# Optimization experiments

Measured on AMD Instinct MI355X. Metric: run time of the kernel, lower is better.

Reference implementation:

```python
import jax, jax.numpy as jnp
import numpy as np

N, C, K = 100000, 64, 27
EPS = 1e-5


def setup_inputs() -> dict:
    key = jax.random.key(0)
    ks = jax.random.split(key, 8)
    feats = jax.random.normal(ks[0], (N, C), dtype=jnp.float32)
    W1 = jax.random.normal(ks[1], (K, C, C), dtype=jnp.float32) * (1.0 / np.sqrt(K * C))
    W2 = jax.random.normal(ks[2], (K, C, C), dtype=jnp.float32) * (1.0 / np.sqrt(K * C))
    gamma1 = jnp.ones((C,), dtype=jnp.float32)
    beta1 = jnp.zeros((C,), dtype=jnp.float32)
    gamma2 = jnp.ones((C,), dtype=jnp.float32)
    beta2 = jnp.zeros((C,), dtype=jnp.float32)
    nbr_idx1 = jax.random.randint(ks[3], (K, N), 0, N, dtype=jnp.int32)
    nbr_idx2 = jax.random.randint(ks[4], (K, N), 0, N, dtype=jnp.int32)
    nbr_mask1 = (jax.random.uniform(ks[5], (K, N)) < 0.7).astype(jnp.float32)
    nbr_mask2 = (jax.random.uniform(ks[6], (K, N)) < 0.7).astype(jnp.float32)
    return {"feats": feats, "W1": W1, "gamma1": gamma1, "beta1": beta1,
            "W2": W2, "gamma2": gamma2, "beta2": beta2,
            "nbr_idx1": nbr_idx1, "nbr_mask1": nbr_mask1,
            "nbr_idx2": nbr_idx2, "nbr_mask2": nbr_mask2}


def sparse_conv(f, idx, mask, W):
    # gather per kernel offset: [K, N, C], mask out missing neighbors
    g = f[idx] * mask[..., None]
    # per-offset GEMM and accumulate over offsets -> [N, C_out]
    return jnp.einsum('knc,kcd->nd', g, W)


def batch_norm(x, gamma, beta):
    # MinkowskiBatchNorm (training): stats over all N points, per channel
    mean = jnp.mean(x, axis=0)
    var = jnp.mean(jnp.square(x - mean), axis=0)
    return (x - mean) * jax.lax.rsqrt(var + EPS) * gamma + beta


def reference(feats, W1, gamma1, beta1, W2, gamma2, beta2,
              nbr_idx1, nbr_mask1, nbr_idx2, nbr_mask2):
    out = sparse_conv(feats, nbr_idx1, nbr_mask1, W1)
    out = jax.nn.relu(batch_norm(out, gamma1, beta1))
    out = sparse_conv(out, nbr_idx2, nbr_mask2, W2)
    out = batch_norm(out, gamma2, beta2)
    out = out + feats          # identity residual (stride=1, no downsample)
    return jax.nn.relu(out)
```

## Files before the change

kernel.cpp:

```cpp
#include <hip/hip_runtime.h>
#include <hip/hip_bf16.h>
#include <stdint.h>
#include <stddef.h>

#define N_PTS 100000
#define KOFF 27

typedef __attribute__((ext_vector_type(8))) __bf16 bf16x8;
typedef __attribute__((ext_vector_type(16))) float f32x16;

__device__ inline unsigned short f2bf(float f) {
  union { float f; unsigned u; } x; x.f = f;
  unsigned r = x.u + 0x7fffu + ((x.u >> 16) & 1u);
  return (unsigned short)(r >> 16);
}

__global__ void fprep_kernel(const float* __restrict__ feats,
                             unsigned short* __restrict__ featsb,
                             unsigned short* __restrict__ f2b,
                             float* __restrict__ stats) {
  int tid = blockIdx.x * blockDim.x + threadIdx.x;
  int stride = gridDim.x * blockDim.x;
  const int NF4 = N_PTS * 16;
  for (int i = tid; i < NF4; i += stride) {
    float4 v = ((const float4*)feats)[i];
    ushort4 o;
    o.x = f2bf(v.x); o.y = f2bf(v.y); o.z = f2bf(v.z); o.w = f2bf(v.w);
    ((ushort4*)featsb)[i] = o;
  }
  if (tid < 256) stats[tid] = 0.f;
  if (tid >= 256 && tid < 264) {
    uint4 z = make_uint4(0u, 0u, 0u, 0u);
    ((uint4*)(featsb + (size_t)N_PTS * 64))[tid - 256] = z;
  }
  if (tid >= 264 && tid < 272) {
    uint4 z = make_uint4(0u, 0u, 0u, 0u);
    ((uint4*)(f2b + (size_t)N_PTS * 64))[tid - 264] = z;
  }
}

__global__ __launch_bounds__(256) void wprep_kernel(const float* __restrict__ W1,
                                                    const float* __restrict__ W2,
                                                    unsigned short* __restrict__ wf1,
                                                    unsigned short* __restrict__ wf2) {
  __shared__ float sW[4096];
  int which = blockIdx.x & 1;
  int k = blockIdx.x >> 1;
  const float* W = (which ? W2 : W1) + (size_t)k * 4096;
  unsigned short* wf = (which ? wf2 : wf1) + (size_t)k * 4096;
  int t = threadIdx.x;
#pragma unroll
  for (int i = 0; i < 4; ++i) {
    ((float4*)sW)[t + 256 * i] = ((const float4*)W)[t + 256 * i];
  }
  __syncthreads();
#pragma unroll
  for (int i = 0; i < 16; ++i) {
    int o = i * 256 + t;
    int j = o & 7, l = (o >> 3) & 63, ct = (o >> 9) & 1, ks = o >> 10;
    int c = ks * 16 + ((l >> 5) << 3) + j;
    int d = (ct << 5) + (l & 31);
    wf[o] = f2bf(sW[c * 64 + d]);
  }
}

#define MFMA(a, b, c) __builtin_amdgcn_mfma_f32_32x32x16_bf16(__builtin_bit_cast(bf16x8, a), __builtin_bit_cast(bf16x8, b), c, 0, 0, 0)

#define STEP(Ac, Bc, An, Bn, giN, mN, giF, mF, kcur)                         \
  {                                                                          \
    int gie = (mN != 0.f) ? giN : N_PTS;                                     \
    const uint4* ar = (const uint4*)(fin + (size_t)gie * 64);                \
    An[0] = ar[hi]; An[1] = ar[2 + hi]; An[2] = ar[4 + hi]; An[3] = ar[6 + hi]; \
    {                                                                        \
      int kn = ((kcur) + 1 <= 26) ? (kcur) + 1 : 26;                         \
      const uint4* bp = wfv + (size_t)kn * 512 + lane;                       \
      Bn[0] = bp[0];   Bn[1] = bp[64];  Bn[2] = bp[128]; Bn[3] = bp[192];    \
      Bn[4] = bp[256]; Bn[5] = bp[320]; Bn[6] = bp[384]; Bn[7] = bp[448];    \
    }                                                                        \
    {                                                                        \
      int kf = ((kcur) + 2 <= 26) ? (kcur) + 2 : 26;                         \
      giF = idxp[kf * N_PTS];                                                \
      float mt = mp[kf * N_PTS];                                             \
      mF = valid ? mt : 0.f;                                                 \
    }                                                                        \
    acc0 = MFMA(Ac[0], Bc[0], acc0);                                         \
    acc1 = MFMA(Ac[0], Bc[1], acc1);                                         \
    acc0 = MFMA(Ac[1], Bc[2], acc0);                                         \
    acc1 = MFMA(Ac[1], Bc[3], acc1);                                         \
    acc0 = MFMA(Ac[2], Bc[4], acc0);                                         \
    acc1 = MFMA(Ac[2], Bc[5], acc1);                                         \
    acc0 = MFMA(Ac[3], Bc[6], acc0);                                         \
    acc1 = MFMA(Ac[3], Bc[7], acc1);                                         \
  }

__global__ __launch_bounds__(256, 3) void conv_kernel(
    const unsigned short* __restrict__ fin,
    const unsigned short* __restrict__ wf,
    const int* __restrict__ idx,
    const float* __restrict__ mask,
    float* __restrict__ yout,
    float* __restrict__ gsum,
    float* __restrict__ gsq)
{
  int lane = threadIdx.x & 63;
  int wid  = threadIdx.x >> 6;
  int col  = lane & 31;
  int hi   = lane >> 5;
  int n0   = blockIdx.x * 128 + wid * 32;
  int n    = n0 + col;
  bool valid = n < N_PTS;
  int nc = valid ? n : (N_PTS - 1);

  const int*   idxp = idx + nc;
  const float* mp   = mask + nc;
  const uint4* wfv  = (const uint4*)wf;

  f32x16 acc0, acc1;
#pragma unroll
  for (int r = 0; r < 16; ++r) { acc0[r] = 0.f; acc1[r] = 0.f; }

  uint4 A0[4], A1[4], B0[8], B1[8];
  int gi0, gi1; float m0, m1;

  gi0 = idxp[0];
  { float mt = mp[0]; m0 = valid ? mt : 0.f; }
  {
    int gie = (m0 != 0.f) ? gi0 : N_PTS;
    const uint4* ar = (const uint4*)(fin + (size_t)gie * 64);
    A0[0] = ar[hi]; A0[1] = ar[2 + hi]; A0[2] = ar[4 + hi]; A0[3] = ar[6 + hi];
    const uint4* bp = wfv + lane;
    B0[0] = bp[0];   B0[1] = bp[64];  B0[2] = bp[128]; B0[3] = bp[192];
    B0[4] = bp[256]; B0[5] = bp[320]; B0[6] = bp[384]; B0[7] = bp[448];
  }
  gi1 = idxp[N_PTS];
  { float mt = mp[N_PTS]; m1 = valid ? mt : 0.f; }

  for (int kk = 0; kk < 13; ++kk) {
    int k = 2 * kk;
    STEP(A0, B0, A1, B1, gi1, m1, gi0, m0, k);
    STEP(A1, B1, A0, B0, gi0, m0, gi1, m1, k + 1);
  }
  acc0 = MFMA(A0[0], B0[0], acc0);
  acc1 = MFMA(A0[0], B0[1], acc1);
  acc0 = MFMA(A0[1], B0[2], acc0);
  acc1 = MFMA(A0[1], B0[3], acc1);
  acc0 = MFMA(A0[2], B0[4], acc0);
  acc1 = MFMA(A0[2], B0[5], acc1);
  acc0 = MFMA(A0[3], B0[6], acc0);
  acc1 = MFMA(A0[3], B0[7], acc1);

  __shared__ float s_sum[64], s_sq[64];
  if (threadIdx.x < 64) { s_sum[threadIdx.x] = 0.f; s_sq[threadIdx.x] = 0.f; }
  __syncthreads();

  float s0 = 0.f, q0 = 0.f, s1 = 0.f, q1 = 0.f;
#pragma unroll
  for (int r = 0; r < 16; ++r) {
    float v = acc0[r]; s0 += v; q0 += v * v;
    float w = acc1[r]; s1 += w; q1 += w * w;
    int rr = (r & 3) + ((r >> 2) << 3) + (hi << 2);
    int nr = n0 + rr;
    if (nr < N_PTS) {
      yout[(size_t)nr * 64 + col]      = v;
      yout[(size_t)nr * 64 + 32 + col] = w;
    }
  }
  atomicAdd(&s_sum[col], s0);
  atomicAdd(&s_sq[col],  q0);
  atomicAdd(&s_sum[32 + col], s1);
  atomicAdd(&s_sq[32 + col],  q1);
  __syncthreads();
  if (threadIdx.x < 64) {
    atomicAdd(&gsum[threadIdx.x], s_sum[threadIdx.x]);
    atomicAdd(&gsq[threadIdx.x],  s_sq[threadIdx.x]);
  }
}

__global__ void bn1_kernel(const float* __restrict__ y,
                           const float* __restrict__ sum,
                           const float* __restrict__ sq,
                           const float* __restrict__ gamma,
                           const float* __restrict__ beta,
                           unsigned short* __restrict__ outb) {
  __shared__ float s_scale[64], s_shift[64];
  if (threadIdx.x < 64) {
    int c = threadIdx.x;
    float mean = sum[c] * (1.f / N_PTS);
    float var  = sq[c] * (1.f / N_PTS) - mean * mean;
    float inv  = rsqrtf(var + 1e-5f);
    float sc   = gamma[c] * inv;
    s_scale[c] = sc;
    s_shift[c] = beta[c] - mean * sc;
  }
  __syncthreads();
  int tid = blockIdx.x * blockDim.x + threadIdx.x;
  int stride = gridDim.x * blockDim.x;
  const int NT = N_PTS * 16;
  for (int i = tid; i < NT; i += stride) {
    float4 v = ((const float4*)y)[i];
    int c = (i * 4) & 63;
    float r0 = fmaxf(v.x * s_scale[c]     + s_shift[c],     0.f);
    float r1 = fmaxf(v.y * s_scale[c + 1] + s_shift[c + 1], 0.f);
    float r2 = fmaxf(v.z * s_scale[c + 2] + s_shift[c + 2], 0.f);
    float r3 = fmaxf(v.w * s_scale[c + 3] + s_shift[c + 3], 0.f);
    ushort4 o;
    o.x = f2bf(r0); o.y = f2bf(r1); o.z = f2bf(r2); o.w = f2bf(r3);
    ((ushort4*)outb)[i] = o;
  }
}

__global__ void bn2_kernel(const float* __restrict__ y,
                           const float* __restrict__ sum,
                           const float* __restrict__ sq,
                           const float* __restrict__ gamma,
                           const float* __restrict__ beta,
                           const float* __restrict__ feats,
                           float* __restrict__ out) {
  __shared__ float s_scale[64], s_shift[64];
  if (threadIdx.x < 64) {
    int c = threadIdx.x;
    float mean = sum[c] * (1.f / N_PTS);
    float var  = sq[c] * (1.f / N_PTS) - mean * mean;
    float inv  = rsqrtf(var + 1e-5f);
    float sc   = gamma[c] * inv;
    s_scale[c] = sc;
    s_shift[c] = beta[c] - mean * sc;
  }
  __syncthreads();
  int tid = blockIdx.x * blockDim.x + threadIdx.x;
  int stride = gridDim.x * blockDim.x;
  const int NT = N_PTS * 16;
  for (int i = tid; i < NT; i += stride) {
    float4 v = ((const float4*)y)[i];
    float4 f = ((const float4*)feats)[i];
    int c = (i * 4) & 63;
    float4 o;
    o.x = fmaxf(v.x * s_scale[c]     + s_shift[c]     + f.x, 0.f);
    o.y = fmaxf(v.y * s_scale[c + 1] + s_shift[c + 1] + f.y, 0.f);
    o.z = fmaxf(v.z * s_scale[c + 2] + s_shift[c + 2] + f.z, 0.f);
    o.w = fmaxf(v.w * s_scale[c + 3] + s_shift[c + 3] + f.w, 0.f);
    ((float4*)out)[i] = o;
  }
}

extern "C" void kernel_launch(void* const* d_in, const int* in_sizes, int n_in,
                              void* d_out, int out_size, void* d_ws, size_t ws_size,
                              hipStream_t stream) {
  const float* feats  = (const float*)d_in[0];
  const float* W1     = (const float*)d_in[1];
  const float* gamma1 = (const float*)d_in[2];
  const float* beta1  = (const float*)d_in[3];
  const float* W2     = (const float*)d_in[4];
  const float* gamma2 = (const float*)d_in[5];
  const float* beta2  = (const float*)d_in[6];
  const int*   idx1   = (const int*)d_in[7];
  const float* mask1  = (const float*)d_in[8];
  const int*   idx2   = (const int*)d_in[9];
  const float* mask2  = (const float*)d_in[10];
  float* out = (float*)d_out;

  char* ws = (char*)d_ws;
  unsigned short* featsb = (unsigned short*)(ws + 0);
  unsigned short* wf1    = (unsigned short*)(ws + 12800768);
  unsigned short* wf2    = (unsigned short*)(ws + 13021952);
  float*          stats  = (float*)(ws + 13243136);
  unsigned short* f2b    = (unsigned short*)(ws + 13244160);

  float* sum1 = stats;       float* sq1 = stats + 64;
  float* sum2 = stats + 128; float* sq2 = stats + 192;

  float* y = out;

  fprep_kernel<<<1024, 256, 0, stream>>>(feats, featsb, f2b, stats);
  wprep_kernel<<<54, 256, 0, stream>>>(W1, W2, wf1, wf2);

  const int CONV_GRID = (N_PTS + 127) / 128;
  conv_kernel<<<CONV_GRID, 256, 0, stream>>>(featsb, wf1, idx1, mask1, y, sum1, sq1);
  bn1_kernel<<<1024, 256, 0, stream>>>(y, sum1, sq1, gamma1, beta1, f2b);
  conv_kernel<<<CONV_GRID, 256, 0, stream>>>(f2b, wf2, idx2, mask2, y, sum2, sq2);
  bn2_kernel<<<1024, 256, 0, stream>>>(y, sum2, sq2, gamma2, beta2, feats, out);
}
```

Measured before the change: 335.1 us.

## Switch conv to 16x16x32 MFMA tiles with 16-point waves and fused prep kernel

```diff
diff --git a/kernel.cpp b/kernel.cpp
--- a/kernel.cpp
+++ b/kernel.cpp
@@ -7,7 +7,7 @@
 #define KOFF 27
 
 typedef __attribute__((ext_vector_type(8))) __bf16 bf16x8;
-typedef __attribute__((ext_vector_type(16))) float f32x16;
+typedef __attribute__((ext_vector_type(4))) float f32x4;
 
 __device__ inline unsigned short f2bf(float f) {
   union { float f; unsigned u; } x; x.f = f;
@@ -15,85 +15,82 @@
   return (unsigned short)(r >> 16);
 }
 
-__global__ void fprep_kernel(const float* __restrict__ feats,
-                             unsigned short* __restrict__ featsb,
-                             unsigned short* __restrict__ f2b,
-                             float* __restrict__ stats) {
-  int tid = blockIdx.x * blockDim.x + threadIdx.x;
-  int stride = gridDim.x * blockDim.x;
+__global__ __launch_bounds__(256) void prep_kernel(const float* __restrict__ feats,
+                                                   const float* __restrict__ W1,
+                                                   const float* __restrict__ W2,
+                                                   unsigned short* __restrict__ featsb,
+                                                   unsigned short* __restrict__ f2b,
+                                                   unsigned short* __restrict__ wf1,
+                                                   unsigned short* __restrict__ wf2,
+                                                   float* __restrict__ stats) {
+  __shared__ float sW[4096];
+  int t = threadIdx.x;
+  if (blockIdx.x < 54) {
+    int which = blockIdx.x & 1;
+    int k = blockIdx.x >> 1;
+    const float* W = (which ? W2 : W1) + (size_t)k * 4096;
+    unsigned short* wf = (which ? wf2 : wf1) + (size_t)k * 4096;
+#pragma unroll
+    for (int i = 0; i < 4; ++i)
+      ((float4*)sW)[t + 256 * i] = ((const float4*)W)[t + 256 * i];
+    __syncthreads();
+#pragma unroll
+    for (int i = 0; i < 16; ++i) {
+      int o = i * 256 + t;
+      int j = o & 7, l = (o >> 3) & 63, nt = (o >> 9) & 3, kk = (o >> 11) & 1;
+      int c = kk * 32 + ((l >> 4) << 3) + j;
+      int d = nt * 16 + (l & 15);
+      wf[o] = f2bf(sW[c * 64 + d]);
+    }
+    return;
+  }
+  int fb = blockIdx.x - 54;
+  int NB = gridDim.x - 54;
   const int NF4 = N_PTS * 16;
-  for (int i = tid; i < NF4; i += stride) {
+  for (int i = fb * 256 + t; i < NF4; i += NB * 256) {
     float4 v = ((const float4*)feats)[i];
     ushort4 o;
     o.x = f2bf(v.x); o.y = f2bf(v.y); o.z = f2bf(v.z); o.w = f2bf(v.w);
     ((ushort4*)featsb)[i] = o;
   }
-  if (tid < 256) stats[tid] = 0.f;
-  if (tid >= 256 && tid < 264) {
+  if (fb == 0) {
+    if (t < 256) stats[t] = 0.f;
     uint4 z = make_uint4(0u, 0u, 0u, 0u);
-    ((uint4*)(featsb + (size_t)N_PTS * 64))[tid - 256] = z;
-  }
-  if (tid >= 264 && tid < 272) {
-    uint4 z = make_uint4(0u, 0u, 0u, 0u);
-    ((uint4*)(f2b + (size_t)N_PTS * 64))[tid - 264] = z;
-  }
-}
-
-__global__ __launch_bounds__(256) void wprep_kernel(const float* __restrict__ W1,
-                                                    const float* __restrict__ W2,
-                                                    unsigned short* __restrict__ wf1,
-                                                    unsigned short* __restrict__ wf2) {
-  __shared__ float sW[4096];
-  int which = blockIdx.x & 1;
-  int k = blockIdx.x >> 1;
-  const float* W = (which ? W2 : W1) + (size_t)k * 4096;
-  unsigned short* wf = (which ? wf2 : wf1) + (size_t)k * 4096;
-  int t = threadIdx.x;
-#pragma unroll
-  for (int i = 0; i < 4; ++i) {
-    ((float4*)sW)[t + 256 * i] = ((const float4*)W)[t + 256 * i];
-  }
-  __syncthreads();
-#pragma unroll
-  for (int i = 0; i < 16; ++i) {
-    int o = i * 256 + t;
-    int j = o & 7, l = (o >> 3) & 63, ct = (o >> 9) & 1, ks = o >> 10;
-    int c = ks * 16 + ((l >> 5) << 3) + j;
-    int d = (ct << 5) + (l & 31);
-    wf[o] = f2bf(sW[c * 64 + d]);
-  }
-}
-
-#define MFMA(a, b, c) __builtin_amdgcn_mfma_f32_32x32x16_bf16(__builtin_bit_cast(bf16x8, a), __builtin_bit_cast(bf16x8, b), c, 0, 0, 0)
-
-#define STEP(Ac, Bc, An, Bn, giN, mN, giF, mF, kcur)                         \
-  {                                                                          \
-    int gie = (mN != 0.f) ? giN : N_PTS;                                     \
-    const uint4* ar = (const uint4*)(fin + (size_t)gie * 64);                \
-    An[0] = ar[hi]; An[1] = ar[2 + hi]; An[2] = ar[4 + hi]; An[3] = ar[6 + hi]; \
-    {                                                                        \
-      int kn = ((kcur) + 1 <= 26) ? (kcur) + 1 : 26;                         \
-      const uint4* bp = wfv + (size_t)kn * 512 + lane;                       \
-      Bn[0] = bp[0];   Bn[1] = bp[64];  Bn[2] = bp[128]; Bn[3] = bp[192];    \
-      Bn[4] = bp[256]; Bn[5] = bp[320]; Bn[6] = bp[384]; Bn[7] = bp[448];    \
-    }                                                                        \
-    {                                                                        \
-      int kf = ((kcur) + 2 <= 26) ? (kcur) + 2 : 26;                         \
-      giF = idxp[kf * N_PTS];                                                \
-      float mt = mp[kf * N_PTS];                                             \
-      mF = valid ? mt : 0.f;                                                 \
-    }                                                                        \
-    acc0 = MFMA(Ac[0], Bc[0], acc0);                                         \
-    acc1 = MFMA(Ac[0], Bc[1], acc1);                                         \
-    acc0 = MFMA(Ac[1], Bc[2], acc0);                                         \
-    acc1 = MFMA(Ac[1], Bc[3], acc1);                                         \
-    acc0 = MFMA(Ac[2], Bc[4], acc0);                                         \
-    acc1 = MFMA(Ac[2], Bc[5], acc1);                                         \
-    acc0 = MFMA(Ac[3], Bc[6], acc0);                                         \
-    acc1 = MFMA(Ac[3], Bc[7], acc1);                                         \
-  }
-
-__global__ __launch_bounds__(256, 3) void conv_kernel(
+    if (t < 8)            ((uint4*)(featsb + (size_t)N_PTS * 64))[t] = z;
+    if (t >= 8 && t < 16) ((uint4*)(f2b    + (size_t)N_PTS * 64))[t - 8] = z;
+  }
+}
+
+#define MFMA16(a, b, c) __builtin_amdgcn_mfma_f32_16x16x32_bf16(__builtin_bit_cast(bf16x8, a), __builtin_bit_cast(bf16x8, b), c, 0, 0, 0)
+
+#define STEP(Ac0, Ac1, An0, An1, giN, mN, giF, mF, kcur)                        \
+  {                                                                             \
+    const uint4* bp = wfv + (size_t)(kcur) * 512 + lane;                        \
+    uint4 b0 = bp[0],   b1 = bp[64],  b2 = bp[128], b3 = bp[192];               \
+    uint4 b4 = bp[256], b5 = bp[320], b6 = bp[384], b7 = bp[448];               \
+    {                                                                           \
+      int gie = (mN != 0.f) ? giN : N_PTS;                                      \
+      const char* rp = (const char*)fin + (size_t)gie * 128 + g16;              \
+      An0 = *(const uint4*)rp;                                                  \
+      An1 = *(const uint4*)(rp + 64);                                           \
+    }                                                                           \
+    {                                                                           \
+      int kf = ((kcur) + 2 <= 26) ? (kcur) + 2 : 26;                            \
+      giF = idxp[(size_t)kf * N_PTS];                                           \
+      float mt = mp[(size_t)kf * N_PTS];                                        \
+      mF = valid ? mt : 0.f;                                                    \
+    }                                                                           \
+    a0 = MFMA16(Ac0, b0, a0);                                                   \
+    a1 = MFMA16(Ac0, b1, a1);                                                   \
+    a2 = MFMA16(Ac0, b2, a2);                                                   \
+    a3 = MFMA16(Ac0, b3, a3);                                                   \
+    a0 = MFMA16(Ac1, b4, a0);                                                   \
+    a1 = MFMA16(Ac1, b5, a1);                                                   \
+    a2 = MFMA16(Ac1, b6, a2);                                                   \
+    a3 = MFMA16(Ac1, b7, a3);                                                   \
+  }
+
+__global__ __launch_bounds__(256, 4) void conv_kernel(
     const unsigned short* __restrict__ fin,
     const unsigned short* __restrict__ wf,
     const int* __restrict__ idx,
@@ -104,10 +101,11 @@
 {
   int lane = threadIdx.x & 63;
   int wid  = threadIdx.x >> 6;
-  int col  = lane & 31;
-  int hi   = lane >> 5;
-  int n0   = blockIdx.x * 128 + wid * 32;
-  int n    = n0 + col;
+  int m    = lane & 15;
+  int g    = lane >> 4;
+  int g16  = g * 16;
+  int n0   = blockIdx.x * 64 + wid * 16;
+  int n    = n0 + m;
   bool valid = n < N_PTS;
   int nc = valid ? n : (N_PTS - 1);
 
@@ -115,60 +113,68 @@
   const float* mp   = mask + nc;
   const uint4* wfv  = (const uint4*)wf;
 
-  f32x16 acc0, acc1;
-#pragma unroll
-  for (int r = 0; r < 16; ++r) { acc0[r] = 0.f; acc1[r] = 0.f; }
-
-  uint4 A0[4], A1[4], B0[8], B1[8];
-  int gi0, gi1; float m0, m1;
-
-  gi0 = idxp[0];
-  { float mt = mp[0]; m0 = valid ? mt : 0.f; }
+  f32x4 a0, a1, a2, a3;
+#pragma unroll
+  for (int r = 0; r < 4; ++r) { a0[r] = 0.f; a1[r] = 0.f; a2[r] = 0.f; a3[r] = 0.f; }
+
+  uint4 Aa0, Aa1, Ab0, Ab1;
+  int gi_a, gi_b; float m_a, m_b;
+
+  gi_a = idxp[0];
+  { float mt = mp[0]; m_a = valid ? mt : 0.f; }
   {
-    int gie = (m0 != 0.f) ? gi0 : N_PTS;
-    const uint4* ar = (const uint4*)(fin + (size_t)gie * 64);
-    A0[0] = ar[hi]; A0[1] = ar[2 + hi]; A0[2] = ar[4 + hi]; A0[3] = ar[6 + hi];
-    const uint4* bp = wfv + lane;
-    B0[0] = bp[0];   B0[1] = bp[64];  B0[2] = bp[128]; B0[3] = bp[192];
-    B0[4] = bp[256]; B0[5] = bp[320]; B0[6] = bp[384]; B0[7] = bp[448];
-  }
-  gi1 = idxp[N_PTS];
-  { float mt = mp[N_PTS]; m1 = valid ? mt : 0.f; }
+    int gie = (m_a != 0.f) ? gi_a : N_PTS;
+    const char* rp = (const char*)fin + (size_t)gie * 128 + g16;
+    Aa0 = *(const uint4*)rp;
+    Aa1 = *(const uint4*)(rp + 64);
+  }
+  gi_b = idxp[N_PTS];
+  { float mt = mp[N_PTS]; m_b = valid ? mt : 0.f; }
 
   for (int kk = 0; kk < 13; ++kk) {
     int k = 2 * kk;
-    STEP(A0, B0, A1, B1, gi1, m1, gi0, m0, k);
-    STEP(A1, B1, A0, B0, gi0, m0, gi1, m1, k + 1);
-  }
-  acc0 = MFMA(A0[0], B0[0], acc0);
-  acc1 = MFMA(A0[0], B0[1], acc1);
-  acc0 = MFMA(A0[1], B0[2], acc0);
-  acc1 = MFMA(A0[1], B0[3], acc1);
-  acc0 = MFMA(A0[2], B0[4], acc0);
-  acc1 = MFMA(A0[2], B0[5], acc1);
-  acc0 = MFMA(A0[3], B0[6], acc0);
-  acc1 = MFMA(A0[3], B0[7], acc1);
+    STEP(Aa0, Aa1, Ab0, Ab1, gi_b, m_b, gi_a, m_a, k);
+    STEP(Ab0, Ab1, Aa0, Aa1, gi_a, m_a, gi_b, m_b, k + 1);
+  }
+  {
+    const uint4* bp = wfv + (size_t)26 * 512 + lane;
+    uint4 b0 = bp[0],   b1 = bp[64],  b2 = bp[128], b3 = bp[192];
+    uint4 b4 = bp[256], b5 = bp[320], b6 = bp[384], b7 = bp[448];
+    a0 = MFMA16(Aa0, b0, a0);
+    a1 = MFMA16(Aa0, b1, a1);
+    a2 = MFMA16(Aa0, b2, a2);
+    a3 = MFMA16(Aa0, b3, a3);
+    a0 = MFMA16(Aa1, b4, a0);
+    a1 = MFMA16(Aa1, b5, a1);
+    a2 = MFMA16(Aa1, b6, a2);
+    a3 = MFMA16(Aa1, b7, a3);
+  }
 
   __shared__ float s_sum[64], s_sq[64];
   if (threadIdx.x < 64) { s_sum[threadIdx.x] = 0.f; s_sq[threadIdx.x] = 0.f; }
   __syncthreads();
 
-  float s0 = 0.f, q0 = 0.f, s1 = 0.f, q1 = 0.f;
-#pragma unroll
-  for (int r = 0; r < 16; ++r) {
-    float v = acc0[r]; s0 += v; q0 += v * v;
-    float w = acc1[r]; s1 += w; q1 += w * w;
-    int rr = (r & 3) + ((r >> 2) << 3) + (hi << 2);
-    int nr = n0 + rr;
-    if (nr < N_PTS) {
-      yout[(size_t)nr * 64 + col]      = v;
-      yout[(size_t)nr * 64 + 32 + col] = w;
+  float s0 = 0.f, q0 = 0.f, s1 = 0.f, q1 = 0.f, s2 = 0.f, q2 = 0.f, s3 = 0.f, q3 = 0.f;
+#pragma unroll
+  for (int r = 0; r < 4; ++r) {
+    int row = n0 + g * 4 + r;
+    bool rv = row < N_PTS;
+    float v0 = a0[r]; s0 += v0; q0 += v0 * v0;
+    float v1 = a1[r]; s1 += v1; q1 += v1 * v1;
+    float v2 = a2[r]; s2 += v2; q2 += v2 * v2;
+    float v3 = a3[r]; s3 += v3; q3 += v3 * v3;
+    if (rv) {
+      float* yr = yout + (size_t)row * 64;
+      yr[m]      = v0;
+      yr[16 + m] = v1;
+      yr[32 + m] = v2;
+      yr[48 + m] = v3;
     }
   }
-  atomicAdd(&s_sum[col], s0);
-  atomicAdd(&s_sq[col],  q0);
-  atomicAdd(&s_sum[32 + col], s1);
-  atomicAdd(&s_sq[32 + col],  q1);
+  atomicAdd(&s_sum[m],      s0); atomicAdd(&s_sq[m],      q0);
+  atomicAdd(&s_sum[16 + m], s1); atomicAdd(&s_sq[16 + m], q1);
+  atomicAdd(&s_sum[32 + m], s2); atomicAdd(&s_sq[32 + m], q2);
+  atomicAdd(&s_sum[48 + m], s3); atomicAdd(&s_sq[48 + m], q3);
   __syncthreads();
   if (threadIdx.x < 64) {
     atomicAdd(&gsum[threadIdx.x], s_sum[threadIdx.x]);
@@ -271,10 +277,9 @@
 
   float* y = out;
 
-  fprep_kernel<<<1024, 256, 0, stream>>>(feats, featsb, f2b, stats);
-  wprep_kernel<<<54, 256, 0, stream>>>(W1, W2, wf1, wf2);
-
-  const int CONV_GRID = (N_PTS + 127) / 128;
+  prep_kernel<<<54 + 640, 256, 0, stream>>>(feats, W1, W2, featsb, f2b, wf1, wf2, stats);
+
+  const int CONV_GRID = (N_PTS + 63) / 64;
   conv_kernel<<<CONV_GRID, 256, 0, stream>>>(featsb, wf1, idx1, mask1, y, sum1, sq1);
   bn1_kernel<<<1024, 256, 0, stream>>>(y, sum1, sq1, gamma1, beta1, f2b);
   conv_kernel<<<CONV_GRID, 256, 0, stream>>>(f2b, wf2, idx2, mask2, y, sum2, sq2);
```

Result: slower. 349.2 us (+4.2%).
